# Kernel optimization log

Measured on AMD Instinct MI355X. Metric: run time of the kernel, lower is better.

Reference implementation:

```python
import jax, jax.numpy as jnp
import numpy as np

D_MODEL = 512
H = 8
D_K = D_MODEL // H


def setup_inputs() -> dict:
    key = jax.random.key(0)
    ks = jax.random.split(key, 11)
    B, S = 2, 4096
    s = 1.0 / np.sqrt(D_MODEL)
    return {
        "q": jax.random.normal(ks[0], (B, S, D_MODEL), jnp.float32),
        "k": jax.random.normal(ks[1], (B, S, D_MODEL), jnp.float32),
        "v": jax.random.normal(ks[2], (B, S, D_MODEL), jnp.float32),
        "w_q": jax.random.normal(ks[3], (D_MODEL, D_MODEL), jnp.float32) * s,
        "b_q": jax.random.normal(ks[4], (D_MODEL,), jnp.float32) * 0.01,
        "w_k": jax.random.normal(ks[5], (D_MODEL, D_MODEL), jnp.float32) * s,
        "b_k": jax.random.normal(ks[6], (D_MODEL,), jnp.float32) * 0.01,
        "w_v": jax.random.normal(ks[7], (D_MODEL, D_MODEL), jnp.float32) * s,
        "b_v": jax.random.normal(ks[8], (D_MODEL,), jnp.float32) * 0.01,
        "w_o": jax.random.normal(ks[9], (D_MODEL, D_MODEL), jnp.float32) * s,
        "b_o": jax.random.normal(ks[10], (D_MODEL,), jnp.float32) * 0.01,
    }


def reference(q, k, v, w_q, b_q, w_k, b_k, w_v, b_v, w_o, b_o):
    B, S, _ = q.shape
    # QKV projections (torch Linear: x @ W.T + b)
    query = q @ w_q.T + b_q
    key_ = k @ w_k.T + b_k
    value = v @ w_v.T + b_v
    # split heads -> [B, H, S, D_K]
    qh = query.reshape(B, S, H, D_K).transpose(0, 2, 1, 3)
    kh = key_.reshape(B, S, H, D_K).transpose(0, 2, 1, 3)
    vh = value.reshape(B, S, H, D_K).transpose(0, 2, 1, 3)
    scores = jnp.einsum('bhsd,bhtd->bhst', qh, kh) / jnp.sqrt(
        jnp.asarray(D_K, qh.dtype))
    attn = jax.nn.softmax(scores, axis=-1)  # dropout = identity in eval
    ctx = jnp.einsum('bhst,bhtd->bhsd', attn, vh)
    out = ctx.transpose(0, 2, 1, 3).reshape(B, S, H * D_K)
    return out @ w_o.T + b_o
```

## Files before the change

### kernel.cpp

```cpp
#include <hip/hip_runtime.h>
#include <hip/hip_bf16.h>


typedef __bf16 bf16_t;
typedef __bf16 bf16x8 __attribute__((ext_vector_type(8)));
typedef __bf16 bf16x4 __attribute__((ext_vector_type(4)));
typedef __bf16 bf16x2 __attribute__((ext_vector_type(2)));
typedef float f32x4 __attribute__((ext_vector_type(4)));
typedef unsigned u32x4 __attribute__((ext_vector_type(4)));

#define S_LEN 4096
#define NH 8
#define DK 64
#define DMODEL 512
#define NB 2
#define KVB 64
#define QB 128

#define EXP2F(x) __builtin_amdgcn_exp2f(x)

__device__ inline void gload_lds16(const void* g, void* l) {
  __builtin_amdgcn_global_load_lds(
      (const __attribute__((address_space(1))) unsigned int*)g,
      (__attribute__((address_space(3))) unsigned int*)l, 16, 0, 0);
}

__device__ inline unsigned pkbf(float a, float b) {
  bf16x2 t; t[0] = (__bf16)a; t[1] = (__bf16)b;
  return __builtin_bit_cast(unsigned, t);
}

__global__ __launch_bounds__(256) void cvt_all(
    const float* __restrict__ q, const float* __restrict__ k,
    const float* __restrict__ v, const float* __restrict__ w0,
    const float* __restrict__ w1, const float* __restrict__ w2,
    const float* __restrict__ w3, bf16_t* __restrict__ x0,
    bf16_t* __restrict__ x1, bf16_t* __restrict__ x2,
    bf16_t* __restrict__ o0, bf16_t* __restrict__ o1,
    bf16_t* __restrict__ o2, bf16_t* __restrict__ o3)
{
  const int bid = blockIdx.x;
  const float* src; bf16_t* dst; int i;
  if (bid < 6144) {
    const int z = bid >> 11;
    src = z == 0 ? q : z == 1 ? k : v;
    dst = z == 0 ? x0 : z == 1 ? x1 : x2;
    i = ((bid & 2047) * 256 + threadIdx.x) * 8;
  } else {
    const int w = (bid - 6144) >> 7;
    src = w == 0 ? w0 : w == 1 ? w1 : w == 2 ? w2 : w3;
    dst = w == 0 ? o0 : w == 1 ? o1 : w == 2 ? o2 : o3;
    i = (((bid - 6144) & 127) * 256 + threadIdx.x) * 8;
  }
  f32x4 a = *reinterpret_cast<const f32x4*>(src + i);
  f32x4 b = *reinterpret_cast<const f32x4*>(src + i + 4);
  bf16x8 r;
#pragma unroll
  for (int j = 0; j < 4; ++j) { r[j] = (__bf16)a[j]; r[j + 4] = (__bf16)b[j]; }
  *reinterpret_cast<bf16x8*>(dst + i) = r;
}

template <typename TO, int NF>
__global__ __launch_bounds__(256) void gemm_tile(
    const bf16_t* __restrict__ A0, const bf16_t* __restrict__ W0,
    const float* __restrict__ bb0, TO* __restrict__ oo0,
    const bf16_t* __restrict__ A1, const bf16_t* __restrict__ W1,
    const float* __restrict__ bb1, TO* __restrict__ oo1,
    const bf16_t* __restrict__ A2, const bf16_t* __restrict__ W2,
    const float* __restrict__ bb2, TO* __restrict__ oo2,
    int mode_last)
{
  const bf16_t* A; const bf16_t* W; const float* bias; TO* out; int mode;
  if (NF == 3) {
    const int z = blockIdx.z;
    if (z == 0)      { A = A0; W = W0; bias = bb0; out = oo0; mode = 0; }
    else if (z == 1) { A = A1; W = W1; bias = bb1; out = oo1; mode = 0; }
    else             { A = A2; W = W2; bias = bb2; out = oo2; mode = 2; }
  } else { A = A0; W = W0; bias = bb0; out = oo0; mode = mode_last; }

  const int mtile = blockIdx.x * 128;
  const int ntile = blockIdx.y * 64;
  const int wave = threadIdx.x >> 6;
  const int lane = threadIdx.x & 63;
  const int l16 = lane & 15;
  const int g = lane >> 4;

  __shared__ bf16_t ldsA[2][128][64];
  __shared__ bf16_t ldsB[2][64][64];

  const int srow8 = 8 * wave + (lane >> 3);
  const int sslot = (lane & 7) ^ ((lane >> 3) & 7);
  const char* Asrc = (const char*)A + ((size_t)(mtile + srow8) * DMODEL) * 2 + sslot * 16;
  const char* Bsrc = (const char*)W + ((size_t)(ntile + srow8) * DMODEL) * 2 + sslot * 16;
  const size_t rblk = (size_t)32 * DMODEL * 2;

  f32x4 acc[2][4];
#pragma unroll
  for (int mb = 0; mb < 2; ++mb)
#pragma unroll
    for (int nb = 0; nb < 4; ++nb) acc[mb][nb] = (f32x4){0.f, 0.f, 0.f, 0.f};

  const int rxor = (l16 & 7) << 4;

#pragma unroll
  for (int c = 0; c < 4; ++c)
    gload_lds16(Asrc + c * rblk, (char*)&ldsA[0][c * 32 + 8 * wave][0]);
#pragma unroll
  for (int c = 0; c < 2; ++c)
    gload_lds16(Bsrc + c * rblk, (char*)&ldsB[0][c * 32 + 8 * wave][0]);
  __syncthreads();

  const int NSTEP = DMODEL / 64;
  int buf = 0;
  for (int t = 0; t < NSTEP; ++t) {
    if (t + 1 < NSTEP) {
      const size_t ko = (size_t)(t + 1) * 128;
#pragma unroll
      for (int c = 0; c < 4; ++c)
        gload_lds16(Asrc + c * rblk + ko, (char*)&ldsA[buf ^ 1][c * 32 + 8 * wave][0]);
#pragma unroll
      for (int c = 0; c < 2; ++c)
        gload_lds16(Bsrc + c * rblk + ko, (char*)&ldsB[buf ^ 1][c * 32 + 8 * wave][0]);
    }

#pragma unroll
    for (int ks = 0; ks < 2; ++ks) {
      bf16x8 af[2];
#pragma unroll
      for (int mb = 0; mb < 2; ++mb) {
        const int arow = wave * 32 + mb * 16 + l16;
        af[mb] = *reinterpret_cast<const bf16x8*>(
            (const char*)&ldsA[buf][0][0] + arow * 128 + ((ks * 64 + g * 16) ^ rxor));
      }
#pragma unroll
      for (int nb = 0; nb < 4; ++nb) {
        const int brow = nb * 16 + l16;
        bf16x8 bfr = *reinterpret_cast<const bf16x8*>(
            (const char*)&ldsB[buf][0][0] + brow * 128 + ((ks * 64 + g * 16) ^ rxor));
#pragma unroll
        for (int mb = 0; mb < 2; ++mb)
          acc[mb][nb] = __builtin_amdgcn_mfma_f32_16x16x32_bf16(af[mb], bfr, acc[mb][nb], 0, 0, 0);
      }
    }

    __syncthreads();
    buf ^= 1;
  }

#pragma unroll
  for (int mb = 0; mb < 2; ++mb) {
    const int m0 = mtile + wave * 32 + mb * 16;
#pragma unroll
    for (int nb = 0; nb < 4; ++nb) {
      const int n = ntile + nb * 16 + l16;
      const float bv = bias[n];
#pragma unroll
      for (int r = 0; r < 4; ++r) {
        const int m = m0 + g * 4 + r;
        float vv = acc[mb][nb][r] + bv;
        size_t addr;
        if (mode == 0) {
          int b = m >> 12, s = m & (S_LEN - 1);
          int h = n >> 6, d = n & 63;
          addr = (((size_t)(b * NH + h) * S_LEN) + s) * DK + d;
        } else if (mode == 2) {
          int b = m >> 12, s = m & (S_LEN - 1);
          int h = n >> 6, d = n & 63;
          addr = (((size_t)(b * NH + h) * DK) + d) * S_LEN + s;
        } else {
          addr = (size_t)m * DMODEL + n;
        }
        out[addr] = (TO)vv;
      }
    }
  }
}

__global__ __launch_bounds__(512) void attn_kernel(
    const bf16_t* __restrict__ Qh, const bf16_t* __restrict__ Kh,
    const bf16_t* __restrict__ Vt, bf16_t* __restrict__ ctx)
{
  const int wg = blockIdx.x;
  const int bh = (wg & 7) * 2 + ((wg >> 3) & 1);
  const int qtile = wg >> 4;
  const int b = bh >> 3, h = bh & 7;
  const int wave = threadIdx.x >> 6;
  const int lane = threadIdx.x & 63;
  const int l16 = lane & 15;
  const int g = lane >> 4;

  __shared__ bf16_t ldsK[2][KVB][64];
  __shared__ bf16_t ldsV[2][KVB][64];

  const bf16_t* Qp = Qh + (size_t)bh * S_LEN * DK;
  const bf16_t* Kp = Kh + (size_t)bh * S_LEN * DK;
  const bf16_t* Vp = Vt + (size_t)bh * DK * S_LEN;

  const int qrow0 = qtile * QB + wave * 16;

  const int srow = 8 * wave + (lane >> 3);
  const int scol16 = (lane & 7) ^ (lane >> 3);
  const char* Ksrc = (const char*)Kp + (size_t)srow * 128 + scol16 * 16;
  const char* Vsrc = (const char*)Vp + (size_t)srow * (S_LEN * 2) + scol16 * 16;

  const float qscale = 0.125f * 1.44269504089f;
  bf16x8 qf[2];
#pragma unroll
  for (int ks = 0; ks < 2; ++ks) {
    bf16x8 t = *reinterpret_cast<const bf16x8*>(
        Qp + (size_t)(qrow0 + l16) * DK + ks * 32 + g * 8);
#pragma unroll
    for (int j = 0; j < 8; ++j) t[j] = (__bf16)((float)t[j] * qscale);
    qf[ks] = t;
  }

  f32x4 o[4];
#pragma unroll
  for (int db = 0; db < 4; ++db) o[db] = (f32x4){0.f, 0.f, 0.f, 0.f};
  float l_run = 0.f;

  const int rxor = (l16 & 7) << 4;

  gload_lds16(Ksrc, (char*)&ldsK[0][8 * wave][0]);
  gload_lds16(Vsrc, (char*)&ldsV[0][8 * wave][0]);
  __syncthreads();

  const int NT = S_LEN / KVB;

#define TILE_BODY(BUF, T)                                                     \
  {                                                                           \
    const int tt = (T);                                                       \
    if (tt + 1 < NT) {                                                        \
      const size_t koff = (size_t)(tt + 1) * (KVB * 128);                     \
      const size_t voff = (size_t)(tt + 1) * (KVB * 2);                       \
      gload_lds16(Ksrc + koff, (char*)&ldsK[(BUF) ^ 1][8 * wave][0]);         \
      gload_lds16(Vsrc + voff, (char*)&ldsV[(BUF) ^ 1][8 * wave][0]);         \
    }                                                                         \
    f32x4 sc[4];                                                              \
    __builtin_amdgcn_s_setprio(1);                                            \
    _Pragma("unroll")                                                         \
    for (int nb = 0; nb < 4; ++nb) {                                          \
      f32x4 a = (f32x4){0.f, 0.f, 0.f, 0.f};                                  \
      _Pragma("unroll")                                                       \
      for (int ks = 0; ks < 2; ++ks) {                                        \
        const int row = nb * 16 + l16;                                        \
        bf16x8 kf = *reinterpret_cast<const bf16x8*>(                         \
            (const char*)&ldsK[BUF][0][0] + row * 128 +                       \
            ((ks * 64 + g * 16) ^ rxor));                                     \
        a = __builtin_amdgcn_mfma_f32_16x16x32_bf16(kf, qf[ks], a, 0, 0, 0);  \
      }                                                                       \
      sc[nb] = a;                                                             \
    }                                                                         \
    __builtin_amdgcn_s_setprio(0);                                            \
    unsigned Wp[4][2];                                                        \
    _Pragma("unroll")                                                         \
    for (int nb = 0; nb < 4; ++nb) {                                          \
      const float p0 = EXP2F(sc[nb][0]);                                      \
      const float p1 = EXP2F(sc[nb][1]);                                      \
      const float p2 = EXP2F(sc[nb][2]);                                      \
      const float p3 = EXP2F(sc[nb][3]);                                      \
      l_run += (p0 + p1) + (p2 + p3);                                         \
      Wp[nb][0] = pkbf(p0, p1);                                               \
      Wp[nb][1] = pkbf(p2, p3);                                               \
    }                                                                         \
    bf16x8 pf[2];                                                             \
    _Pragma("unroll")                                                         \
    for (int ks = 0; ks < 2; ++ks) {                                          \
      unsigned x0 = Wp[2 * ks][0], y0 = Wp[2 * ks + 1][0];                    \
      unsigned x1 = Wp[2 * ks][1], y1 = Wp[2 * ks + 1][1];                    \
      asm("v_permlane32_swap_b32 %0, %1" : "+v"(x0), "+v"(y0));               \
      asm("v_permlane16_swap_b32 %0, %1" : "+v"(x0), "+v"(y0));               \
      asm("v_permlane32_swap_b32 %0, %1" : "+v"(x1), "+v"(y1));               \
      asm("v_permlane16_swap_b32 %0, %1" : "+v"(x1), "+v"(y1));               \
      u32x4 pw4 = (u32x4){x0, x1, y0, y1};                                    \
      pf[ks] = __builtin_bit_cast(bf16x8, pw4);                               \
    }                                                                         \
    __builtin_amdgcn_s_setprio(1);                                            \
    _Pragma("unroll")                                                         \
    for (int ks = 0; ks < 2; ++ks) {                                          \
      _Pragma("unroll")                                                       \
      for (int db = 0; db < 4; ++db) {                                        \
        const int row = db * 16 + l16;                                        \
        bf16x8 vf = *reinterpret_cast<const bf16x8*>(                         \
            (const char*)&ldsV[BUF][0][0] + row * 128 +                       \
            ((ks * 64 + g * 16) ^ rxor));                                     \
        o[db] = __builtin_amdgcn_mfma_f32_16x16x32_bf16(vf, pf[ks], o[db], 0, 0, 0); \
      }                                                                       \
    }                                                                         \
    __builtin_amdgcn_s_setprio(0);                                            \
    __syncthreads();                                                          \
  }

  for (int t = 0; t < NT; t += 2) {
    TILE_BODY(0, t)
    TILE_BODY(1, t + 1)
  }
#undef TILE_BODY

  float l_row = l_run;
  l_row += __shfl_xor(l_row, 16);
  l_row += __shfl_xor(l_row, 32);
  const float inv_l = 1.f / l_row;
  bf16_t* crow = ctx + (((size_t)(b * S_LEN + qrow0 + l16)) * NH + h) * DK;
#pragma unroll
  for (int db = 0; db < 4; ++db) {
    bf16x4 cw;
#pragma unroll
    for (int r = 0; r < 4; ++r) cw[r] = (__bf16)(o[db][r] * inv_l);
    *reinterpret_cast<bf16x4*>(crow + db * 16 + g * 4) = cw;
  }
}

extern "C" void kernel_launch(void* const* d_in, const int* in_sizes, int n_in,
                              void* d_out, int out_size, void* d_ws, size_t ws_size,
                              hipStream_t stream)
{
  const float* q   = (const float*)d_in[0];
  const float* k   = (const float*)d_in[1];
  const float* v   = (const float*)d_in[2];
  const float* w_q = (const float*)d_in[3];
  const float* b_q = (const float*)d_in[4];
  const float* w_k = (const float*)d_in[5];
  const float* b_k = (const float*)d_in[6];
  const float* w_v = (const float*)d_in[7];
  const float* b_v = (const float*)d_in[8];
  const float* w_o = (const float*)d_in[9];
  const float* b_o = (const float*)d_in[10];
  float* out = (float*)d_out;

  char* ws = (char*)d_ws;
  const size_t sz = (size_t)NB * NH * S_LEN * DK * sizeof(bf16_t);
  const size_t wsz = (size_t)DMODEL * DMODEL * sizeof(bf16_t);
  bf16_t* X0 = (bf16_t*)(ws);
  bf16_t* X1 = (bf16_t*)(ws + sz);
  bf16_t* X2 = (bf16_t*)(ws + 2 * sz);
  bf16_t* Qh = (bf16_t*)(ws + 3 * sz);
  bf16_t* Kh = (bf16_t*)(ws + 4 * sz);
  bf16_t* Wq = (bf16_t*)(ws + 5 * sz);
  bf16_t* Wk = (bf16_t*)(ws + 5 * sz + wsz);
  bf16_t* Wv = (bf16_t*)(ws + 5 * sz + 2 * wsz);
  bf16_t* Wo = (bf16_t*)(ws + 5 * sz + 3 * wsz);
  bf16_t* Vt  = X0;
  bf16_t* ctx = X1;

  cvt_all<<<dim3(6656), 256, 0, stream>>>(q, k, v, w_q, w_k, w_v, w_o,
                                          X0, X1, X2, Wq, Wk, Wv, Wo);

  dim3 bb(256);
  gemm_tile<bf16_t, 3><<<dim3(64, 8, 3), bb, 0, stream>>>(
      X0, Wq, b_q, Qh, X1, Wk, b_k, Kh, X2, Wv, b_v, Vt, 0);

  attn_kernel<<<dim3(512), dim3(512), 0, stream>>>(Qh, Kh, Vt, ctx);

  gemm_tile<float, 1><<<dim3(64, 8), bb, 0, stream>>>(
      ctx, Wo, b_o, out, nullptr, nullptr, nullptr, nullptr,
      nullptr, nullptr, nullptr, nullptr, 1);
}
```

Baseline: 138.0 us.

## Fuse fp32-to-bf16 input conversion into QKV projection GEMM A-tile loads

Removes the separate conversion of q/k/v to bf16 and instead has the QKV GEMM load fp32 A tiles into registers, convert them, and write them swizzled into LDS, while weights are still pre-converted by a smaller kernel. This is meant to eliminate a full write and re-read of the bf16 activation copies plus one launch. In exchange, the GEMM reads twice as many bytes per A tile across its N-tile blocks, and the A path loses direct global-to-LDS loads, now using register staging with a register-held prefetch.

Measured after the change: 140.7 us. No clear change (+1.9%).

```diff
diff --git a/kernel.cpp b/kernel.cpp
--- a/kernel.cpp
+++ b/kernel.cpp
@@ -30,47 +30,40 @@
   return __builtin_bit_cast(unsigned, t);
 }
 
-__global__ __launch_bounds__(256) void cvt_all(
-    const float* __restrict__ q, const float* __restrict__ k,
-    const float* __restrict__ v, const float* __restrict__ w0,
-    const float* __restrict__ w1, const float* __restrict__ w2,
-    const float* __restrict__ w3, bf16_t* __restrict__ x0,
-    bf16_t* __restrict__ x1, bf16_t* __restrict__ x2,
+__device__ inline bf16x8 cvt8(f32x4 lo, f32x4 hi) {
+  bf16x8 r;
+#pragma unroll
+  for (int j = 0; j < 4; ++j) { r[j] = (__bf16)lo[j]; r[j + 4] = (__bf16)hi[j]; }
+  return r;
+}
+
+__global__ __launch_bounds__(256) void cvt_w(
+    const float* __restrict__ w0, const float* __restrict__ w1,
+    const float* __restrict__ w2, const float* __restrict__ w3,
     bf16_t* __restrict__ o0, bf16_t* __restrict__ o1,
     bf16_t* __restrict__ o2, bf16_t* __restrict__ o3)
 {
-  const int bid = blockIdx.x;
-  const float* src; bf16_t* dst; int i;
-  if (bid < 6144) {
-    const int z = bid >> 11;
-    src = z == 0 ? q : z == 1 ? k : v;
-    dst = z == 0 ? x0 : z == 1 ? x1 : x2;
-    i = ((bid & 2047) * 256 + threadIdx.x) * 8;
-  } else {
-    const int w = (bid - 6144) >> 7;
-    src = w == 0 ? w0 : w == 1 ? w1 : w == 2 ? w2 : w3;
-    dst = w == 0 ? o0 : w == 1 ? o1 : w == 2 ? o2 : o3;
-    i = (((bid - 6144) & 127) * 256 + threadIdx.x) * 8;
-  }
+  const float* src = blockIdx.y == 0 ? w0 : blockIdx.y == 1 ? w1
+                   : blockIdx.y == 2 ? w2 : w3;
+  bf16_t* dst = blockIdx.y == 0 ? o0 : blockIdx.y == 1 ? o1
+              : blockIdx.y == 2 ? o2 : o3;
+  const int i = (blockIdx.x * 256 + threadIdx.x) * 8;
   f32x4 a = *reinterpret_cast<const f32x4*>(src + i);
   f32x4 b = *reinterpret_cast<const f32x4*>(src + i + 4);
-  bf16x8 r;
-#pragma unroll
-  for (int j = 0; j < 4; ++j) { r[j] = (__bf16)a[j]; r[j + 4] = (__bf16)b[j]; }
-  *reinterpret_cast<bf16x8*>(dst + i) = r;
-}
-
-template <typename TO, int NF>
+  *reinterpret_cast<bf16x8*>(dst + i) = cvt8(a, b);
+}
+
+template <typename TA, typename TO, int NF>
 __global__ __launch_bounds__(256) void gemm_tile(
-    const bf16_t* __restrict__ A0, const bf16_t* __restrict__ W0,
+    const TA* __restrict__ A0, const bf16_t* __restrict__ W0,
     const float* __restrict__ bb0, TO* __restrict__ oo0,
-    const bf16_t* __restrict__ A1, const bf16_t* __restrict__ W1,
+    const TA* __restrict__ A1, const bf16_t* __restrict__ W1,
     const float* __restrict__ bb1, TO* __restrict__ oo1,
-    const bf16_t* __restrict__ A2, const bf16_t* __restrict__ W2,
+    const TA* __restrict__ A2, const bf16_t* __restrict__ W2,
     const float* __restrict__ bb2, TO* __restrict__ oo2,
     int mode_last)
 {
-  const bf16_t* A; const bf16_t* W; const float* bias; TO* out; int mode;
+  const TA* A; const bf16_t* W; const float* bias; TO* out; int mode;
   if (NF == 3) {
     const int z = blockIdx.z;
     if (z == 0)      { A = A0; W = W0; bias = bb0; out = oo0; mode = 0; }
@@ -90,7 +83,6 @@
 
   const int srow8 = 8 * wave + (lane >> 3);
   const int sslot = (lane & 7) ^ ((lane >> 3) & 7);
-  const char* Asrc = (const char*)A + ((size_t)(mtile + srow8) * DMODEL) * 2 + sslot * 16;
   const char* Bsrc = (const char*)W + ((size_t)(ntile + srow8) * DMODEL) * 2 + sslot * 16;
   const size_t rblk = (size_t)32 * DMODEL * 2;
 
@@ -101,51 +93,107 @@
     for (int nb = 0; nb < 4; ++nb) acc[mb][nb] = (f32x4){0.f, 0.f, 0.f, 0.f};
 
   const int rxor = (l16 & 7) << 4;
-
-#pragma unroll
-  for (int c = 0; c < 4; ++c)
-    gload_lds16(Asrc + c * rblk, (char*)&ldsA[0][c * 32 + 8 * wave][0]);
-#pragma unroll
-  for (int c = 0; c < 2; ++c)
-    gload_lds16(Bsrc + c * rblk, (char*)&ldsB[0][c * 32 + 8 * wave][0]);
-  __syncthreads();
-
   const int NSTEP = DMODEL / 64;
-  int buf = 0;
-  for (int t = 0; t < NSTEP; ++t) {
-    if (t + 1 < NSTEP) {
-      const size_t ko = (size_t)(t + 1) * 128;
-#pragma unroll
-      for (int c = 0; c < 4; ++c)
-        gload_lds16(Asrc + c * rblk + ko, (char*)&ldsA[buf ^ 1][c * 32 + 8 * wave][0]);
-#pragma unroll
-      for (int c = 0; c < 2; ++c)
-        gload_lds16(Bsrc + c * rblk + ko, (char*)&ldsB[buf ^ 1][c * 32 + 8 * wave][0]);
+
+#define GEMM_MFMA(BUFX)                                                       \
+  {                                                                           \
+    _Pragma("unroll")                                                         \
+    for (int ks = 0; ks < 2; ++ks) {                                          \
+      bf16x8 af[2];                                                           \
+      _Pragma("unroll")                                                       \
+      for (int mb = 0; mb < 2; ++mb) {                                        \
+        const int arow = wave * 32 + mb * 16 + l16;                           \
+        af[mb] = *reinterpret_cast<const bf16x8*>(                            \
+            (const char*)&ldsA[BUFX][0][0] + arow * 128 +                     \
+            ((ks * 64 + g * 16) ^ rxor));                                     \
+      }                                                                       \
+      _Pragma("unroll")                                                       \
+      for (int nb = 0; nb < 4; ++nb) {                                        \
+        const int brow = nb * 16 + l16;                                       \
+        bf16x8 bfr = *reinterpret_cast<const bf16x8*>(                        \
+            (const char*)&ldsB[BUFX][0][0] + brow * 128 +                     \
+            ((ks * 64 + g * 16) ^ rxor));                                     \
+        _Pragma("unroll")                                                     \
+        for (int mb = 0; mb < 2; ++mb)                                        \
+          acc[mb][nb] = __builtin_amdgcn_mfma_f32_16x16x32_bf16(              \
+              af[mb], bfr, acc[mb][nb], 0, 0, 0);                             \
+      }                                                                       \
+    }                                                                         \
+  }
+
+  if constexpr (sizeof(TA) == 4) {
+    const float* abase[4];
+    int wrow[4], wslot[4];
+#pragma unroll
+    for (int u = 0; u < 4; ++u) {
+      const int idx = threadIdx.x + 256 * u;
+      const int row = idx >> 3, slot = idx & 7;
+      wrow[u] = row; wslot[u] = slot;
+      const int sc = slot ^ (row & 7);
+      abase[u] = (const float*)A + (size_t)(mtile + row) * DMODEL + sc * 8;
     }
-
-#pragma unroll
-    for (int ks = 0; ks < 2; ++ks) {
-      bf16x8 af[2];
-#pragma unroll
-      for (int mb = 0; mb < 2; ++mb) {
-        const int arow = wave * 32 + mb * 16 + l16;
-        af[mb] = *reinterpret_cast<const bf16x8*>(
-            (const char*)&ldsA[buf][0][0] + arow * 128 + ((ks * 64 + g * 16) ^ rxor));
+    f32x4 ra[4][2];
+
+#define LOAD_A(T)                                                             \
+    _Pragma("unroll")                                                         \
+    for (int u = 0; u < 4; ++u) {                                             \
+      ra[u][0] = *reinterpret_cast<const f32x4*>(abase[u] + (T) * 64);        \
+      ra[u][1] = *reinterpret_cast<const f32x4*>(abase[u] + (T) * 64 + 4);    \
+    }
+#define WRITE_A(BUFX)                                                         \
+    _Pragma("unroll")                                                         \
+    for (int u = 0; u < 4; ++u)                                               \
+      *reinterpret_cast<bf16x8*>(&ldsA[BUFX][wrow[u]][wslot[u] * 8]) =        \
+          cvt8(ra[u][0], ra[u][1]);
+
+    LOAD_A(0);
+#pragma unroll
+    for (int c = 0; c < 2; ++c)
+      gload_lds16(Bsrc + c * rblk, (char*)&ldsB[0][c * 32 + 8 * wave][0]);
+
+    for (int t = 0; t < NSTEP; ++t) {
+      const int buf = t & 1;
+      WRITE_A(buf);
+      __syncthreads();
+      if (t + 1 < NSTEP) {
+        LOAD_A(t + 1);
+        const size_t ko = (size_t)(t + 1) * 128;
+#pragma unroll
+        for (int c = 0; c < 2; ++c)
+          gload_lds16(Bsrc + c * rblk + ko,
+                      (char*)&ldsB[buf ^ 1][c * 32 + 8 * wave][0]);
       }
-#pragma unroll
-      for (int nb = 0; nb < 4; ++nb) {
-        const int brow = nb * 16 + l16;
-        bf16x8 bfr = *reinterpret_cast<const bf16x8*>(
-            (const char*)&ldsB[buf][0][0] + brow * 128 + ((ks * 64 + g * 16) ^ rxor));
-#pragma unroll
-        for (int mb = 0; mb < 2; ++mb)
-          acc[mb][nb] = __builtin_amdgcn_mfma_f32_16x16x32_bf16(af[mb], bfr, acc[mb][nb], 0, 0, 0);
+      GEMM_MFMA(buf)
+    }
+#undef LOAD_A
+#undef WRITE_A
+  } else {
+    const char* Asrc = (const char*)A + ((size_t)(mtile + srow8) * DMODEL) * 2 + sslot * 16;
+#pragma unroll
+    for (int c = 0; c < 4; ++c)
+      gload_lds16(Asrc + c * rblk, (char*)&ldsA[0][c * 32 + 8 * wave][0]);
+#pragma unroll
+    for (int c = 0; c < 2; ++c)
+      gload_lds16(Bsrc + c * rblk, (char*)&ldsB[0][c * 32 + 8 * wave][0]);
+    __syncthreads();
+
+    int buf = 0;
+    for (int t = 0; t < NSTEP; ++t) {
+      if (t + 1 < NSTEP) {
+        const size_t ko = (size_t)(t + 1) * 128;
+#pragma unroll
+        for (int c = 0; c < 4; ++c)
+          gload_lds16(Asrc + c * rblk + ko, (char*)&ldsA[buf ^ 1][c * 32 + 8 * wave][0]);
+#pragma unroll
+        for (int c = 0; c < 2; ++c)
+          gload_lds16(Bsrc + c * rblk + ko, (char*)&ldsB[buf ^ 1][c * 32 + 8 * wave][0]);
       }
+      GEMM_MFMA(buf)
+      __syncthreads();
+      buf ^= 1;
     }
-
-    __syncthreads();
-    buf ^= 1;
-  }
+  }
+#undef GEMM_MFMA
 
 #pragma unroll
   for (int mb = 0; mb < 2; ++mb) {
@@ -331,28 +379,24 @@
   char* ws = (char*)d_ws;
   const size_t sz = (size_t)NB * NH * S_LEN * DK * sizeof(bf16_t);
   const size_t wsz = (size_t)DMODEL * DMODEL * sizeof(bf16_t);
-  bf16_t* X0 = (bf16_t*)(ws);
-  bf16_t* X1 = (bf16_t*)(ws + sz);
-  bf16_t* X2 = (bf16_t*)(ws + 2 * sz);
-  bf16_t* Qh = (bf16_t*)(ws + 3 * sz);
-  bf16_t* Kh = (bf16_t*)(ws + 4 * sz);
-  bf16_t* Wq = (bf16_t*)(ws + 5 * sz);
-  bf16_t* Wk = (bf16_t*)(ws + 5 * sz + wsz);
-  bf16_t* Wv = (bf16_t*)(ws + 5 * sz + 2 * wsz);
-  bf16_t* Wo = (bf16_t*)(ws + 5 * sz + 3 * wsz);
-  bf16_t* Vt  = X0;
-  bf16_t* ctx = X1;
-
-  cvt_all<<<dim3(6656), 256, 0, stream>>>(q, k, v, w_q, w_k, w_v, w_o,
-                                          X0, X1, X2, Wq, Wk, Wv, Wo);
+  bf16_t* ctx = (bf16_t*)(ws);
+  bf16_t* Qh  = (bf16_t*)(ws + sz);
+  bf16_t* Kh  = (bf16_t*)(ws + 2 * sz);
+  bf16_t* Vt  = (bf16_t*)(ws + 3 * sz);
+  bf16_t* Wq  = (bf16_t*)(ws + 4 * sz);
+  bf16_t* Wk  = (bf16_t*)(ws + 4 * sz + wsz);
+  bf16_t* Wv  = (bf16_t*)(ws + 4 * sz + 2 * wsz);
+  bf16_t* Wo  = (bf16_t*)(ws + 4 * sz + 3 * wsz);
+
+  cvt_w<<<dim3(128, 4), 256, 0, stream>>>(w_q, w_k, w_v, w_o, Wq, Wk, Wv, Wo);
 
   dim3 bb(256);
-  gemm_tile<bf16_t, 3><<<dim3(64, 8, 3), bb, 0, stream>>>(
-      X0, Wq, b_q, Qh, X1, Wk, b_k, Kh, X2, Wv, b_v, Vt, 0);
+  gemm_tile<float, bf16_t, 3><<<dim3(64, 8, 3), bb, 0, stream>>>(
+      q, Wq, b_q, Qh, k, Wk, b_k, Kh, v, Wv, b_v, Vt, 0);
 
   attn_kernel<<<dim3(512), dim3(512), 0, stream>>>(Qh, Kh, Vt, ctx);
 
-  gemm_tile<float, 1><<<dim3(64, 8), bb, 0, stream>>>(
+  gemm_tile<bf16_t, float, 1><<<dim3(64, 8), bb, 0, stream>>>(
       ctx, Wo, b_o, out, nullptr, nullptr, nullptr, nullptr,
       nullptr, nullptr, nullptr, nullptr, 1);
 }
```
